# Kernel optimization log

Hardware: AMD Instinct MI355X
Metric: run time of the kernel (lower is better)

Reference implementation:

```python
import jax, jax.numpy as jnp
import numpy as np

B, S, H = 32, 64, 512
ATT = 128


def _window_index_tables(seq_len):
    # Enumerate all contiguous windows of size 2..S, same set (order-independent
    # for the softmax-weighted sum) as the torch double loop.
    starts, ends = [], []
    for w in range(2, seq_len + 1):
        for s in range(0, seq_len - w + 1):
            starts.append(s)
            ends.append(s + w)
    starts = np.asarray(starts, np.int32)
    ends = np.asarray(ends, np.int32)
    widths = ends - starts
    ks = np.floor(np.log2(widths)).astype(np.int32)  # sparse-table level per window
    e2 = ends - (1 << ks)                            # second gather position
    return starts, e2, ks


def setup_inputs() -> dict:
    key = jax.random.key(0)
    k0, k1, k2, k3, k4 = jax.random.split(key, 5)
    return {
        "lstm_out": jax.random.normal(k0, (B, S, H), dtype=jnp.float32),
        "W1": jax.random.normal(k1, (H, ATT), dtype=jnp.float32) * 0.05,
        "b1": jax.random.normal(k2, (ATT,), dtype=jnp.float32) * 0.05,
        "W2": jax.random.normal(k3, (ATT, 1), dtype=jnp.float32) * 0.05,
        "b2": jax.random.normal(k4, (1,), dtype=jnp.float32) * 0.05,
    }


def reference(lstm_out, W1, b1, W2, b2):
    b, s, h = lstm_out.shape
    # Sparse table: M[k][:, i] = max over lstm_out[:, i : i+2^k] (clipped to s).
    n_levels = int(np.floor(np.log2(s))) + 1
    tables = [lstm_out]
    for k in range(1, n_levels):
        half = 1 << (k - 1)
        prev = tables[-1]
        shifted = jnp.concatenate(
            [prev[:, half:], jnp.full((b, half, h), -jnp.inf, prev.dtype)], axis=1)
        tables.append(jnp.maximum(prev, shifted))
    Mstack = jnp.stack(tables)  # [K, B, S, H]

    starts, e2, ks = _window_index_tables(s)
    # Range max of each window = max of two overlapping power-of-two blocks.
    pooled = jnp.maximum(Mstack[ks, :, starts], Mstack[ks, :, e2])  # [n_win, B, H]
    pooled = jnp.transpose(pooled, (1, 0, 2))  # [B, n_win, H]

    hid = jax.nn.relu(jnp.einsum("bnh,ha->bna", pooled, W1) + b1)
    scores = jnp.einsum("bna,ao->bno", hid, W2) + b2  # [B, n_win, 1]
    attn = jax.nn.softmax(scores, axis=1)
    return jnp.sum(attn * pooled, axis=1)  # [B, H]
```

## Files before the change

kernel.cpp:

```cpp
#include <hip/hip_runtime.h>
#include <stdint.h>


typedef unsigned short u16;
typedef unsigned int u32;

#define B_    32
#define S_    64
#define H_    512
#define ATT_  128
#define NWIN  2016
#define NLEV  7
#define TLEV  6

typedef __bf16 bf16x8 __attribute__((ext_vector_type(8)));
typedef float  f32x4  __attribute__((ext_vector_type(4)));

__device__ __forceinline__ float asf(u32 i) {
  union { u32 i; float f; } v; v.i = i; return v.f;
}
__device__ __forceinline__ u32 asu(float f) {
  union { float f; u32 i; } v; v.f = f; return v.i;
}
__device__ __forceinline__ float bf2f(u16 u) { return asf(((u32)u) << 16); }
__device__ __forceinline__ u16 f2bf(float f) {
  u32 i = asu(f);
  i += 0x7fffu + ((i >> 16) & 1u);
  return (u16)(i >> 16);
}
__device__ __forceinline__ u32 bfmax2(u32 a, u32 b) {
  float a0 = asf(a << 16), a1 = asf(a & 0xffff0000u);
  float b0 = asf(b << 16), b1 = asf(b & 0xffff0000u);
  u32 m0 = asu(fmaxf(a0, b0)), m1 = asu(fmaxf(a1, b1));
  return (m1 & 0xffff0000u) | (m0 >> 16);
}
__device__ __forceinline__ uint4 bfmax8(uint4 a, uint4 b) {
  uint4 m;
  m.x = bfmax2(a.x, b.x); m.y = bfmax2(a.y, b.y);
  m.z = bfmax2(a.z, b.z); m.w = bfmax2(a.w, b.w);
  return m;
}
__device__ __forceinline__ bf16x8 as_bf16x8(uint4 v) {
  union { uint4 u; bf16x8 h; } c; c.u = v; return c.h;
}

__launch_bounds__(256)
__global__ void k01_init(const float* __restrict__ lstm, const float* __restrict__ W1,
                         u16* __restrict__ table, u16* __restrict__ w1t,
                         u16* __restrict__ widx) {
  int bid = blockIdx.x, tid = threadIdx.x;
  __shared__ u16 bufA[64 * 64], bufB[64 * 64];
  if (bid < 256) {
    int hc = bid & 7, b = bid >> 3;
    const float* src = lstm + (size_t)b * S_ * H_ + hc * 64;
    u16* tb = table + (size_t)b * TLEV * S_ * H_ + hc * 64;
    for (int t = tid; t < 64 * 16; t += 256) {
      int r = t >> 4, c4 = t & 15;
      float4 f = *reinterpret_cast<const float4*>(src + r * H_ + c4 * 4);
      ushort4 u;
      u.x = f2bf(f.x); u.y = f2bf(f.y); u.z = f2bf(f.z); u.w = f2bf(f.w);
      *reinterpret_cast<ushort4*>(&bufA[r * 64 + c4 * 4]) = u;
    }
    u16* pa = bufA; u16* pb = bufB;
    for (int k = 1; k < NLEV; ++k) {
      __syncthreads();
      int half = 1 << (k - 1);
      u16* dst_g = tb + (size_t)(k - 1) * S_ * H_;
      for (int t = tid; t < 64 * 16; t += 256) {
        int r = t >> 4, c4 = t & 15;
        int r2 = r + half; if (r2 > 63) r2 = 63;
        uint2 a  = *reinterpret_cast<const uint2*>(&pa[r  * 64 + c4 * 4]);
        uint2 bq = *reinterpret_cast<const uint2*>(&pa[r2 * 64 + c4 * 4]);
        uint2 m; m.x = bfmax2(a.x, bq.x); m.y = bfmax2(a.y, bq.y);
        *reinterpret_cast<uint2*>(&pb[r * 64 + c4 * 4]) = m;
        *reinterpret_cast<uint2*>(dst_g + r * H_ + c4 * 4) = m;
      }
      u16* tmp = pa; pa = pb; pb = tmp;
    }
  } else {
    int gb = bid - 256;
    if (gb == 0) {
      for (int n = tid; n < NWIN; n += 256) {
        int w = 2, rem = n;
        while (rem >= 65 - w) { rem -= 65 - w; ++w; }
        int s = rem;
        int k = 31 - __clz(w);
        int e2 = s + w - (1 << k);
        widx[n] = (u16)(s | (e2 << 6) | (k << 12));
      }
    }
    for (int q = tid; q < 2048; q += 256) {
      int idx = gb * 2048 + q;
      int n = idx >> 9, kq = idx & 511;
      w1t[idx] = f2bf(W1[kq * ATT_ + n]);
    }
  }
}

__launch_bounds__(256)
__attribute__((amdgpu_waves_per_eu(1, 4)))
__global__ void k2_scores(const u16* __restrict__ table, const u16* __restrict__ w1t,
                          const float* __restrict__ b1, const float* __restrict__ w2,
                          const u16* __restrict__ widx, float* __restrict__ scores) {
  const int b = blockIdx.y, mt = blockIdx.x;
  __shared__ u16 Ts[128 * 64];
  __shared__ u16 Bs[128 * 64];
  __shared__ u16 widx_l[64];
  __shared__ float b1s[128], w2s[128];
  int tid = threadIdx.x;
  if (tid < 64) {
    int n = mt * 64 + tid; if (n > NWIN - 1) n = NWIN - 1;
    widx_l[tid] = widx[n];
  }
  if (tid < 128) { b1s[tid] = b1[tid]; w2s[tid] = w2[tid]; }
  __syncthreads();

  const int lv_lo = widx_l[0] >> 12;
  const u16* tb = table + (size_t)b * TLEV * S_ * H_ + (size_t)(lv_lo - 1) * S_ * H_;

  int t0 = tid, t1 = tid + 256, t2 = tid + 512, t3 = tid + 768;
  int r0 = t0 >> 3, r1 = t1 >> 3, r2 = t2 >> 3, r3 = t3 >> 3;
  int c0 = t0 & 7,  c1 = t1 & 7,  c2 = t2 & 7,  c3 = t3 & 7;
  const u16* ts0 = tb + r0 * H_ + c0 * 8;
  const u16* ts1 = tb + r1 * H_ + c1 * 8;
  const u16* ts2 = tb + r2 * H_ + c2 * 8;
  const u16* ts3 = tb + r3 * H_ + c3 * 8;
  const u16* bs0 = w1t + r0 * H_ + c0 * 8;
  const u16* bs1 = w1t + r1 * H_ + c1 * 8;
  const u16* bs2 = w1t + r2 * H_ + c2 * 8;
  const u16* bs3 = w1t + r3 * H_ + c3 * 8;
  int sd0 = r0 * 64 + ((c0 ^ (r0 & 7)) * 8);
  int sd1 = r1 * 64 + ((c1 ^ (r1 & 7)) * 8);
  int sd2 = r2 * 64 + ((c2 ^ (r2 & 7)) * 8);
  int sd3 = r3 * 64 + ((c3 ^ (r3 & 7)) * 8);

  int wid = tid >> 6, lane = tid & 63;
  int lrow = lane & 15, quad = lane >> 4;

  int aoff[2][2];
  {
    int pk = widx_l[wid * 16 + lrow];
    int s = pk & 63, e2 = (pk >> 6) & 63, lv = (pk >> 12) - lv_lo;
    int rs = lv * 64 + s, re = lv * 64 + e2;
#pragma unroll
    for (int k2i = 0; k2i < 2; ++k2i) {
      int c = quad + k2i * 4;
      aoff[k2i][0] = rs * 64 + ((c ^ (rs & 7)) * 8);
      aoff[k2i][1] = re * 64 + ((c ^ (re & 7)) * 8);
    }
  }
  int boff[8][2];
#pragma unroll
  for (int j = 0; j < 8; ++j) {
    int n = j * 16 + lrow;
#pragma unroll
    for (int k2i = 0; k2i < 2; ++k2i) {
      int c = quad + k2i * 4;
      boff[j][k2i] = n * 64 + ((c ^ (n & 7)) * 8);
    }
  }

  uint4 rT0, rT1, rT2, rT3, rB0, rB1, rB2, rB3;

#define ISSUE(KK) do { \
  rT0 = *reinterpret_cast<const uint4*>(ts0 + (KK)); \
  rT1 = *reinterpret_cast<const uint4*>(ts1 + (KK)); \
  rT2 = *reinterpret_cast<const uint4*>(ts2 + (KK)); \
  rT3 = *reinterpret_cast<const uint4*>(ts3 + (KK)); \
  rB0 = *reinterpret_cast<const uint4*>(bs0 + (KK)); \
  rB1 = *reinterpret_cast<const uint4*>(bs1 + (KK)); \
  rB2 = *reinterpret_cast<const uint4*>(bs2 + (KK)); \
  rB3 = *reinterpret_cast<const uint4*>(bs3 + (KK)); \
} while (0)

#define STAGE() do { \
  *reinterpret_cast<uint4*>(&Ts[sd0]) = rT0; \
  *reinterpret_cast<uint4*>(&Ts[sd1]) = rT1; \
  *reinterpret_cast<uint4*>(&Ts[sd2]) = rT2; \
  *reinterpret_cast<uint4*>(&Ts[sd3]) = rT3; \
  *reinterpret_cast<uint4*>(&Bs[sd0]) = rB0; \
  *reinterpret_cast<uint4*>(&Bs[sd1]) = rB1; \
  *reinterpret_cast<uint4*>(&Bs[sd2]) = rB2; \
  *reinterpret_cast<uint4*>(&Bs[sd3]) = rB3; \
} while (0)

  ISSUE(0);

  f32x4 acc[8];
#pragma unroll
  for (int j = 0; j < 8; ++j) acc[j] = (f32x4){0.f, 0.f, 0.f, 0.f};

  for (int kc = 0; kc < 7; ++kc) {
    __syncthreads();
    STAGE();
    __syncthreads();
    ISSUE((kc + 1) * 64);
#pragma unroll
    for (int k2i = 0; k2i < 2; ++k2i) {
      uint4 va = *reinterpret_cast<const uint4*>(&Ts[aoff[k2i][0]]);
      uint4 vb = *reinterpret_cast<const uint4*>(&Ts[aoff[k2i][1]]);
      bf16x8 af = as_bf16x8(bfmax8(va, vb));
#pragma unroll
      for (int j = 0; j < 8; ++j) {
        bf16x8 bfr = *reinterpret_cast<const bf16x8*>(&Bs[boff[j][k2i]]);
        acc[j] = __builtin_amdgcn_mfma_f32_16x16x32_bf16(af, bfr, acc[j], 0, 0, 0);
      }
    }
  }
  __syncthreads();
  STAGE();
  __syncthreads();
#pragma unroll
  for (int k2i = 0; k2i < 2; ++k2i) {
    uint4 va = *reinterpret_cast<const uint4*>(&Ts[aoff[k2i][0]]);
    uint4 vb = *reinterpret_cast<const uint4*>(&Ts[aoff[k2i][1]]);
    bf16x8 af = as_bf16x8(bfmax8(va, vb));
#pragma unroll
    for (int j = 0; j < 8; ++j) {
      bf16x8 bfr = *reinterpret_cast<const bf16x8*>(&Bs[boff[j][k2i]]);
      acc[j] = __builtin_amdgcn_mfma_f32_16x16x32_bf16(af, bfr, acc[j], 0, 0, 0);
    }
  }

#undef ISSUE
#undef STAGE

#pragma unroll
  for (int r = 0; r < 4; ++r) {
    float p = 0.f;
#pragma unroll
    for (int j = 0; j < 8; ++j) {
      int n = j * 16 + lrow;
      float v = acc[j][r] + b1s[n];
      p += (v > 0.f ? v : 0.f) * w2s[n];
    }
    p += __shfl_xor(p, 1, 16);
    p += __shfl_xor(p, 2, 16);
    p += __shfl_xor(p, 4, 16);
    p += __shfl_xor(p, 8, 16);
    if (lrow == 0) {
      int nw = mt * 64 + wid * 16 + quad * 4 + r;
      if (nw < NWIN) scores[b * NWIN + nw] = p;
    }
  }
}

__launch_bounds__(256)
__global__ void k34_out(const u16* __restrict__ table, const float* __restrict__ scores,
                        const u16* __restrict__ widx, float* __restrict__ out) {
  int hc = blockIdx.x, b = blockIdx.y, tid = threadIdx.x;
  __shared__ u16 Tl[6 * 64 * 32];
  __shared__ float attn_l[NWIN];
  __shared__ u16 widx_l[NWIN];
  __shared__ float red[8][32];
  __shared__ float wredM[4], wredS[4];
  const u16* tb = table + (size_t)b * TLEV * S_ * H_;
  int h0 = hc * 32;
  int lane = tid & 63, wid = tid >> 6;

  for (int t = tid; t < 6 * 64 * 4; t += 256) {
    int row = t >> 2, c = t & 3;
    uint4 v = *reinterpret_cast<const uint4*>(tb + row * H_ + h0 + c * 8);
    *reinterpret_cast<uint4*>(&Tl[row * 32 + c * 8]) = v;
  }
  for (int n = tid; n < NWIN; n += 256) widx_l[n] = widx[n];

  float mx = -1e30f;
  for (int n = tid; n < NWIN; n += 256) {
    float v = scores[b * NWIN + n];
    attn_l[n] = v;
    mx = fmaxf(mx, v);
  }
#pragma unroll
  for (int off = 32; off > 0; off >>= 1) mx = fmaxf(mx, __shfl_xor(mx, off, 64));
  if (lane == 0) wredM[wid] = mx;
  __syncthreads();
  mx = fmaxf(fmaxf(wredM[0], wredM[1]), fmaxf(wredM[2], wredM[3]));
  float sum = 0.f;
  for (int n = tid; n < NWIN; n += 256) {
    float e = __expf(attn_l[n] - mx);
    attn_l[n] = e;
    sum += e;
  }
#pragma unroll
  for (int off = 32; off > 0; off >>= 1) sum += __shfl_xor(sum, off, 64);
  if (lane == 0) wredS[wid] = sum;
  __syncthreads();
  float inv = 1.f / (wredS[0] + wredS[1] + wredS[2] + wredS[3]);

  int h = tid & 31, g = tid >> 5;
  float acc = 0.f;
  for (int n = g * 252; n < g * 252 + 252; ++n) {
    int pk = widx_l[n];
    int s = pk & 63, e2 = (pk >> 6) & 63, lv = pk >> 12;
    float va = bf2f(Tl[((lv - 1) * 64 + s) * 32 + h]);
    float vb = bf2f(Tl[((lv - 1) * 64 + e2) * 32 + h]);
    acc += attn_l[n] * fmaxf(va, vb);
  }
  red[g][h] = acc;
  __syncthreads();
  if (tid < 32) {
    float s2 = 0.f;
#pragma unroll
    for (int g2 = 0; g2 < 8; ++g2) s2 += red[g2][tid];
    out[b * H_ + h0 + tid] = s2 * inv;
  }
}

extern "C" void kernel_launch(void* const* d_in, const int* in_sizes, int n_in,
                              void* d_out, int out_size, void* d_ws, size_t ws_size,
                              hipStream_t stream) {
  const float* lstm = (const float*)d_in[0];
  const float* W1   = (const float*)d_in[1];
  const float* b1   = (const float*)d_in[2];
  const float* W2   = (const float*)d_in[3];
  float* out = (float*)d_out;

  char* ws = (char*)d_ws;
  u16*   widx   = (u16*)(ws + 0);
  u16*   w1t    = (u16*)(ws + 4096);
  u16*   table  = (u16*)(ws + 135168);
  float* scores = (float*)(ws + 12718080);

  k01_init <<<288, 256, 0, stream>>>(lstm, W1, table, w1t, widx);
  k2_scores<<<dim3(32, B_), 256, 0, stream>>>(table, w1t, b1, W2, widx, scores);
  k34_out  <<<dim3(16, B_), 256, 0, stream>>>(table, scores, widx, out);
}
```

Measured before the change: 116.6 us.

## Load GEMM operands directly from global memory instead of LDS staging

```diff
diff --git a/kernel.cpp b/kernel.cpp
--- a/kernel.cpp
+++ b/kernel.cpp
@@ -103,8 +103,6 @@
                           const float* __restrict__ b1, const float* __restrict__ w2,
                           const u16* __restrict__ widx, float* __restrict__ scores) {
   const int b = blockIdx.y, mt = blockIdx.x;
-  __shared__ u16 Ts[128 * 64];
-  __shared__ u16 Bs[128 * 64];
   __shared__ u16 widx_l[64];
   __shared__ float b1s[128], w2s[128];
   int tid = threadIdx.x;
@@ -115,115 +113,39 @@
   if (tid < 128) { b1s[tid] = b1[tid]; w2s[tid] = w2[tid]; }
   __syncthreads();
 
-  const int lv_lo = widx_l[0] >> 12;
-  const u16* tb = table + (size_t)b * TLEV * S_ * H_ + (size_t)(lv_lo - 1) * S_ * H_;
-
-  int t0 = tid, t1 = tid + 256, t2 = tid + 512, t3 = tid + 768;
-  int r0 = t0 >> 3, r1 = t1 >> 3, r2 = t2 >> 3, r3 = t3 >> 3;
-  int c0 = t0 & 7,  c1 = t1 & 7,  c2 = t2 & 7,  c3 = t3 & 7;
-  const u16* ts0 = tb + r0 * H_ + c0 * 8;
-  const u16* ts1 = tb + r1 * H_ + c1 * 8;
-  const u16* ts2 = tb + r2 * H_ + c2 * 8;
-  const u16* ts3 = tb + r3 * H_ + c3 * 8;
-  const u16* bs0 = w1t + r0 * H_ + c0 * 8;
-  const u16* bs1 = w1t + r1 * H_ + c1 * 8;
-  const u16* bs2 = w1t + r2 * H_ + c2 * 8;
-  const u16* bs3 = w1t + r3 * H_ + c3 * 8;
-  int sd0 = r0 * 64 + ((c0 ^ (r0 & 7)) * 8);
-  int sd1 = r1 * 64 + ((c1 ^ (r1 & 7)) * 8);
-  int sd2 = r2 * 64 + ((c2 ^ (r2 & 7)) * 8);
-  int sd3 = r3 * 64 + ((c3 ^ (r3 & 7)) * 8);
+  const u16* tbB = table + (size_t)b * TLEV * S_ * H_;
 
   int wid = tid >> 6, lane = tid & 63;
   int lrow = lane & 15, quad = lane >> 4;
 
-  int aoff[2][2];
-  {
-    int pk = widx_l[wid * 16 + lrow];
-    int s = pk & 63, e2 = (pk >> 6) & 63, lv = (pk >> 12) - lv_lo;
-    int rs = lv * 64 + s, re = lv * 64 + e2;
-#pragma unroll
-    for (int k2i = 0; k2i < 2; ++k2i) {
-      int c = quad + k2i * 4;
-      aoff[k2i][0] = rs * 64 + ((c ^ (rs & 7)) * 8);
-      aoff[k2i][1] = re * 64 + ((c ^ (re & 7)) * 8);
-    }
-  }
-  int boff[8][2];
-#pragma unroll
-  for (int j = 0; j < 8; ++j) {
-    int n = j * 16 + lrow;
-#pragma unroll
-    for (int k2i = 0; k2i < 2; ++k2i) {
-      int c = quad + k2i * 4;
-      boff[j][k2i] = n * 64 + ((c ^ (n & 7)) * 8);
-    }
-  }
-
-  uint4 rT0, rT1, rT2, rT3, rB0, rB1, rB2, rB3;
-
-#define ISSUE(KK) do { \
-  rT0 = *reinterpret_cast<const uint4*>(ts0 + (KK)); \
-  rT1 = *reinterpret_cast<const uint4*>(ts1 + (KK)); \
-  rT2 = *reinterpret_cast<const uint4*>(ts2 + (KK)); \
-  rT3 = *reinterpret_cast<const uint4*>(ts3 + (KK)); \
-  rB0 = *reinterpret_cast<const uint4*>(bs0 + (KK)); \
-  rB1 = *reinterpret_cast<const uint4*>(bs1 + (KK)); \
-  rB2 = *reinterpret_cast<const uint4*>(bs2 + (KK)); \
-  rB3 = *reinterpret_cast<const uint4*>(bs3 + (KK)); \
-} while (0)
-
-#define STAGE() do { \
-  *reinterpret_cast<uint4*>(&Ts[sd0]) = rT0; \
-  *reinterpret_cast<uint4*>(&Ts[sd1]) = rT1; \
-  *reinterpret_cast<uint4*>(&Ts[sd2]) = rT2; \
-  *reinterpret_cast<uint4*>(&Ts[sd3]) = rT3; \
-  *reinterpret_cast<uint4*>(&Bs[sd0]) = rB0; \
-  *reinterpret_cast<uint4*>(&Bs[sd1]) = rB1; \
-  *reinterpret_cast<uint4*>(&Bs[sd2]) = rB2; \
-  *reinterpret_cast<uint4*>(&Bs[sd3]) = rB3; \
-} while (0)
-
-  ISSUE(0);
+  int pk = widx_l[wid * 16 + lrow];
+  int s = pk & 63, e2 = (pk >> 6) & 63, lv = pk >> 12;
+  const u16* aS = tbB + (size_t)((lv - 1) * S_ + s)  * H_ + quad * 8;
+  const u16* aE = tbB + (size_t)((lv - 1) * S_ + e2) * H_ + quad * 8;
+  const u16* bp[8];
+#pragma unroll
+  for (int j = 0; j < 8; ++j) bp[j] = w1t + (j * 16 + lrow) * H_ + quad * 8;
 
   f32x4 acc[8];
 #pragma unroll
   for (int j = 0; j < 8; ++j) acc[j] = (f32x4){0.f, 0.f, 0.f, 0.f};
 
-  for (int kc = 0; kc < 7; ++kc) {
-    __syncthreads();
-    STAGE();
-    __syncthreads();
-    ISSUE((kc + 1) * 64);
-#pragma unroll
-    for (int k2i = 0; k2i < 2; ++k2i) {
-      uint4 va = *reinterpret_cast<const uint4*>(&Ts[aoff[k2i][0]]);
-      uint4 vb = *reinterpret_cast<const uint4*>(&Ts[aoff[k2i][1]]);
-      bf16x8 af = as_bf16x8(bfmax8(va, vb));
-#pragma unroll
-      for (int j = 0; j < 8; ++j) {
-        bf16x8 bfr = *reinterpret_cast<const bf16x8*>(&Bs[boff[j][k2i]]);
-        acc[j] = __builtin_amdgcn_mfma_f32_16x16x32_bf16(af, bfr, acc[j], 0, 0, 0);
-      }
-    }
-  }
-  __syncthreads();
-  STAGE();
-  __syncthreads();
-#pragma unroll
-  for (int k2i = 0; k2i < 2; ++k2i) {
-    uint4 va = *reinterpret_cast<const uint4*>(&Ts[aoff[k2i][0]]);
-    uint4 vb = *reinterpret_cast<const uint4*>(&Ts[aoff[k2i][1]]);
-    bf16x8 af = as_bf16x8(bfmax8(va, vb));
+  for (int kc = 0; kc < 8; ++kc) {
+    int kk = kc * 64;
+    uint4 as0 = *reinterpret_cast<const uint4*>(aS + kk);
+    uint4 ae0 = *reinterpret_cast<const uint4*>(aE + kk);
+    uint4 as1 = *reinterpret_cast<const uint4*>(aS + kk + 32);
+    uint4 ae1 = *reinterpret_cast<const uint4*>(aE + kk + 32);
+    bf16x8 af0 = as_bf16x8(bfmax8(as0, ae0));
+    bf16x8 af1 = as_bf16x8(bfmax8(as1, ae1));
 #pragma unroll
     for (int j = 0; j < 8; ++j) {
-      bf16x8 bfr = *reinterpret_cast<const bf16x8*>(&Bs[boff[j][k2i]]);
-      acc[j] = __builtin_amdgcn_mfma_f32_16x16x32_bf16(af, bfr, acc[j], 0, 0, 0);
-    }
-  }
-
-#undef ISSUE
-#undef STAGE
+      bf16x8 b0 = *reinterpret_cast<const bf16x8*>(bp[j] + kk);
+      bf16x8 b1v = *reinterpret_cast<const bf16x8*>(bp[j] + kk + 32);
+      acc[j] = __builtin_amdgcn_mfma_f32_16x16x32_bf16(af0, b0, acc[j], 0, 0, 0);
+      acc[j] = __builtin_amdgcn_mfma_f32_16x16x32_bf16(af1, b1v, acc[j], 0, 0, 0);
+    }
+  }
 
 #pragma unroll
   for (int r = 0; r < 4; ++r) {
```

Measured after the change: 169.3 us. 1.45x slower.
